# Performance work log

Measured on AMD Instinct MI355X. Metric: run time of the kernel, lower is better.

## Reference

```python
import math
import jax, jax.numpy as jnp
import numpy as np

N_HEADS = 16

def setup_inputs() -> dict:
    key = jax.random.key(0)
    ks = jax.random.split(key, 6)
    B, T, D = 2, 4096, 1024
    m, dh = 256, D // N_HEADS
    x = jax.random.normal(ks[0], (B, T, D), dtype=jnp.float32)
    s = 1.0 / math.sqrt(D)
    wq = jax.random.normal(ks[1], (D, D), dtype=jnp.float32) * s
    wk = jax.random.normal(ks[2], (D, D), dtype=jnp.float32) * s
    wv = jax.random.normal(ks[3], (D, D), dtype=jnp.float32) * s
    wo = jax.random.normal(ks[4], (D, D), dtype=jnp.float32) * s
    rf = jax.random.normal(ks[5], (m, dh), dtype=jnp.float32) / math.sqrt(dh)
    return {"x": x, "wq": wq, "wk": wk, "wv": wv, "wo": wo, "rf": rf}

def _phi(x, rf, m):
    # x: [B,H,T,Dh]; rf: [m,Dh] -> phi: [B,H,T,2m]
    norms_sq = jnp.sum(x * x, axis=-1, keepdims=True)            # [B,H,T,1]
    proj = jnp.einsum('bhtd,md->bhtm', x, rf)                     # [B,H,T,m]
    scale = jnp.exp(-norms_sq * 0.5) / math.sqrt(m)
    return jnp.concatenate([jnp.cos(proj), jnp.sin(proj)], axis=-1) * scale

def reference(x, wq, wk, wv, wo, rf):
    B, T, D = x.shape
    H = N_HEADS
    Dh = D // H
    m = rf.shape[0]
    def heads(w):
        return (x @ w.T).reshape(B, T, H, Dh).transpose(0, 2, 1, 3)  # [B,H,T,Dh]
    Q, K, V = heads(wq), heads(wk), heads(wv)
    Qf = _phi(Q, rf, m)                                            # [B,H,T,2m]
    Kf = _phi(K, rf, m)
    KV = jnp.einsum('bhnd,bhnv->bhdv', Kf, V)                      # [B,H,2m,Dh]
    QKV = jnp.einsum('bhnd,bhdv->bhnv', Qf, KV)                    # [B,H,T,Dh]
    K_sum = jnp.sum(Kf, axis=2)                                    # [B,H,2m]
    Z = jnp.maximum(jnp.einsum('bhnd,bhd->bhn', Qf, K_sum)[..., None], 1e-6)
    out = (QKV / Z).transpose(0, 2, 1, 3).reshape(B, T, D)
    return out @ wo.T
```

## Files before the change

kernel.cpp:

```cpp
#include <hip/hip_runtime.h>


#define TSEQ  4096
#define BSZ   2
#define BT    8192
#define DM    1024
#define NHEAD 16
#define DHEAD 64
#define FF    512

typedef __attribute__((ext_vector_type(8))) __bf16 bf16x8;
typedef __attribute__((ext_vector_type(4))) __bf16 bf16x4;
typedef __attribute__((ext_vector_type(4))) float floatx4;

#define MFMA_BF16(a, b, c) __builtin_amdgcn_mfma_f32_16x16x32_bf16(a, b, c, 0, 0, 0)

__device__ __forceinline__ void load_lds_16B(const void* g, void* l) {
    __builtin_amdgcn_global_load_lds(
        (const __attribute__((address_space(1))) void*)g,
        (__attribute__((address_space(3))) void*)l, 16, 0, 0);
}

__global__ __launch_bounds__(256) void split2_kernel(
    const float* __restrict__ src, __bf16* __restrict__ hi, __bf16* __restrict__ lo, int n4)
{
    int i = blockIdx.x * 256 + threadIdx.x;
    if (i >= n4) return;
    float4 v = ((const float4*)src)[i];
    bf16x4 h = {(__bf16)v.x, (__bf16)v.y, (__bf16)v.z, (__bf16)v.w};
    bf16x4 l = {(__bf16)(v.x - (float)h[0]), (__bf16)(v.y - (float)h[1]),
                (__bf16)(v.z - (float)h[2]), (__bf16)(v.w - (float)h[3])};
    ((bf16x4*)hi)[i] = h;
    ((bf16x4*)lo)[i] = l;
}

__global__ __launch_bounds__(256) void split1_kernel(
    const float* __restrict__ src, __bf16* __restrict__ hi, int n4)
{
    int i = blockIdx.x * 256 + threadIdx.x;
    if (i >= n4) return;
    float4 v = ((const float4*)src)[i];
    bf16x4 h = {(__bf16)v.x, (__bf16)v.y, (__bf16)v.z, (__bf16)v.w};
    ((bf16x4*)hi)[i] = h;
}

template<bool SPLIT, int EPI>
__global__ __launch_bounds__(256, 2)
void gemm_mfma_kernel(const __bf16* __restrict__ Ahi, const __bf16* __restrict__ Alo,
                      const __bf16* __restrict__ Whi, const __bf16* __restrict__ Wlo,
                      float* __restrict__ Cf, __bf16* __restrict__ Cb,
                      float* __restrict__ norms)
{
    __shared__ __bf16 As[SPLIT ? 2 : 1][128 * 32];
    __shared__ __bf16 Bs[SPLIT ? 2 : 1][128 * 32];

    const int t = threadIdx.x;
    const int bm = blockIdx.y * 128, bn = blockIdx.x * 128;
    const int lane = t & 63, mth = lane & 15, q = lane >> 4, wave = t >> 6;
    const int wrow = (wave & 1) * 64, wcol = (wave >> 1) * 64;
    const int qsw = q ^ ((mth >> 1) & 3);
    const int csw = (t & 3) ^ ((t >> 3) & 3);

    const size_t arow = (size_t)(bm + (t >> 2)) * DM + csw * 8;
    const size_t brow = (size_t)(bn + (t >> 2)) * DM + csw * 8;
    const int l0 = t * 8;
    const int l1 = 64 * 32 + t * 8;

    floatx4 acc[4][4];
#pragma unroll
    for (int i = 0; i < 4; ++i)
#pragma unroll
        for (int j = 0; j < 4; ++j) acc[i][j] = (floatx4){0.f, 0.f, 0.f, 0.f};

    for (int k0 = 0; k0 < DM; k0 += 32) {
        __syncthreads();
        load_lds_16B(Ahi + arow + k0,             &As[0][l0]);
        load_lds_16B(Ahi + arow + 64 * DM + k0,   &As[0][l1]);
        load_lds_16B(Whi + brow + k0,             &Bs[0][l0]);
        load_lds_16B(Whi + brow + 64 * DM + k0,   &Bs[0][l1]);
        if (SPLIT) {
            load_lds_16B(Alo + arow + k0,           &As[1][l0]);
            load_lds_16B(Alo + arow + 64 * DM + k0, &As[1][l1]);
            load_lds_16B(Wlo + brow + k0,           &Bs[1][l0]);
            load_lds_16B(Wlo + brow + 64 * DM + k0, &Bs[1][l1]);
        }
        __syncthreads();

        bf16x8 ah[4], bh[4], al[4], bl[4];
#pragma unroll
        for (int i = 0; i < 4; ++i) {
            ah[i] = *(const bf16x8*)&As[0][(wrow + i * 16 + mth) * 32 + qsw * 8];
            bh[i] = *(const bf16x8*)&Bs[0][(wcol + i * 16 + mth) * 32 + qsw * 8];
        }
        if (SPLIT) {
#pragma unroll
            for (int i = 0; i < 4; ++i) {
                al[i] = *(const bf16x8*)&As[1][(wrow + i * 16 + mth) * 32 + qsw * 8];
                bl[i] = *(const bf16x8*)&Bs[1][(wcol + i * 16 + mth) * 32 + qsw * 8];
            }
        }
#pragma unroll
        for (int i = 0; i < 4; ++i)
#pragma unroll
            for (int j = 0; j < 4; ++j) {
                acc[i][j] = MFMA_BF16(ah[i], bh[j], acc[i][j]);
                if (SPLIT) {
                    acc[i][j] = MFMA_BF16(ah[i], bl[j], acc[i][j]);
                    acc[i][j] = MFMA_BF16(al[i], bh[j], acc[i][j]);
                }
            }
    }

    if (EPI == 2) {
        const int head = (bn + wcol) >> 6;
#pragma unroll
        for (int i = 0; i < 4; ++i)
#pragma unroll
            for (int r = 0; r < 4; ++r) {
                float s = acc[i][0][r] * acc[i][0][r] + acc[i][1][r] * acc[i][1][r]
                        + acc[i][2][r] * acc[i][2][r] + acc[i][3][r] * acc[i][3][r];
                s += __shfl_xor(s, 1); s += __shfl_xor(s, 2);
                s += __shfl_xor(s, 4); s += __shfl_xor(s, 8);
                if (mth == 0)
                    norms[(size_t)head * BT + (bm + wrow + i * 16 + q * 4 + r)] = s;
            }
    }
    if (EPI == 3) {
#pragma unroll
        for (int i = 0; i < 4; ++i)
#pragma unroll
            for (int j = 0; j < 4; ++j) {
                const int cg = bn + wcol + j * 16 + mth;
                const int hh = cg >> 6, vloc = cg & 63;
                const int r0 = bm + wrow + i * 16 + q * 4;
                const int bb = r0 >> 12, tloc = r0 & 4095;
                bf16x4 w = {(__bf16)acc[i][j][0], (__bf16)acc[i][j][1],
                            (__bf16)acc[i][j][2], (__bf16)acc[i][j][3]};
                *(bf16x4*)(Cb + ((size_t)(bb * 16 + hh) * 64 + vloc) * TSEQ + tloc) = w;
            }
        return;
    }
#pragma unroll
    for (int i = 0; i < 4; ++i)
#pragma unroll
        for (int r = 0; r < 4; ++r) {
            const size_t gr = (size_t)(bm + wrow + i * 16 + q * 4 + r) * DM
                            + bn + wcol + mth;
            if (EPI == 0) {
#pragma unroll
                for (int j = 0; j < 4; ++j) Cf[gr + j * 16] = acc[i][j][r];
            } else {
#pragma unroll
                for (int j = 0; j < 4; ++j) Cb[gr + j * 16] = (__bf16)acc[i][j][r];
            }
        }
}

__global__ __launch_bounds__(256, 3)
void kv_mfma_kernel(const __bf16* __restrict__ Kb, const __bf16* __restrict__ Vt,
                    const float* __restrict__ Knorm,
                    const __bf16* __restrict__ rfh_g, const __bf16* __restrict__ rfl_g,
                    float* __restrict__ KVpart)
{
    __shared__ __bf16 rfh[4096], rfl[4096], Kc[4096], VtS[5120], phiT[8192];
    __shared__ float scaleS[64];

    const int fb = blockIdx.x, bh = blockIdx.y, z = blockIdx.z;
    const int b = bh >> 4, h = bh & 15;
    const int tid = threadIdx.x, wave = tid >> 6, lane = tid & 63;
    const int m = lane & 15, q = lane >> 4;
    const int lr = lane >> 2;
    const int csw = (lane & 3) ^ ((lr >> 1) & 3);
    const int qsw = q ^ ((m >> 1) & 3);

#pragma unroll
    for (int L = 0; L < 2; ++L) {
        const int f = wave * 16 + lr, d = L * 32 + csw * 8;
        load_lds_16B(rfh_g + (size_t)(fb * 64 + f) * DHEAD + d,
                     (char*)rfh + L * 4096 + wave * 1024 + lane * 16);
        load_lds_16B(rfl_g + (size_t)(fb * 64 + f) * DHEAD + d,
                     (char*)rfl + L * 4096 + wave * 1024 + lane * 16);
    }
    for (int idx = tid; idx < 1024; idx += 256) {
        const int kt = idx >> 9, rr = (idx >> 5) & 15, cc = idx & 31;
        VtS[kt * 2560 + (64 + rr) * 32 + cc] = (rr == 0) ? (__bf16)1.0f : (__bf16)0.0f;
    }

    floatx4 acc[2][5];
#pragma unroll
    for (int s = 0; s < 2; ++s)
#pragma unroll
        for (int v = 0; v < 5; ++v) acc[s][v] = (floatx4){0.f, 0.f, 0.f, 0.f};

    for (int ch = z * 8; ch < z * 8 + 8; ++ch) {
        __syncthreads();
#pragma unroll
        for (int L = 0; L < 2; ++L) {
            const int tr = wave * 16 + lr, d = L * 32 + csw * 8;
            load_lds_16B(Kb + (size_t)(b * TSEQ + ch * 64 + tr) * DM + h * 64 + d,
                         (char*)Kc + L * 4096 + wave * 1024 + lane * 16);
            load_lds_16B(Vt + ((size_t)bh * 64 + tr) * TSEQ + ch * 64 + d,
                         (char*)VtS + L * 5120 + wave * 1024 + lane * 16);
        }
        if (tid < 64)
            scaleS[tid] = __expf(-0.5f * Knorm[(size_t)h * BT + b * TSEQ + ch * 64 + tid]) * 0.0625f;
        __syncthreads();

        floatx4 pr[4];
#pragma unroll
        for (int ft = 0; ft < 4; ++ft) pr[ft] = (floatx4){0.f, 0.f, 0.f, 0.f};
#pragma unroll
        for (int kt = 0; kt < 2; ++kt) {
            const bf16x8 ka = *(const bf16x8*)(Kc + kt * 2048 + (wave * 16 + m) * 32 + qsw * 8);
#pragma unroll
            for (int ft = 0; ft < 4; ++ft) {
                const bf16x8 yh = *(const bf16x8*)(rfh + kt * 2048 + (ft * 16 + m) * 32 + qsw * 8);
                const bf16x8 yl = *(const bf16x8*)(rfl + kt * 2048 + (ft * 16 + m) * 32 + qsw * 8);
                pr[ft] = MFMA_BF16(ka, yh, pr[ft]);
                pr[ft] = MFMA_BF16(ka, yl, pr[ft]);
            }
        }
        {
            const int pg = wave >> 1;
            const int cph = (wave & 1) * 2 + (q >> 1);
            const int sub8 = (q & 1) * 8;
#pragma unroll
            for (int ft = 0; ft < 4; ++ft) {
                const int fo = ft * 16 + m;
                bf16x4 pc, ps;
#pragma unroll
                for (int r = 0; r < 4; ++r) {
                    const float sc = scaleS[wave * 16 + q * 4 + r];
                    float sv, cv;
                    __sincosf(pr[ft][r], &sv, &cv);
                    pc[r] = (__bf16)(cv * sc);
                    ps[r] = (__bf16)(sv * sc);
                }
                const int off = pg * 8192 + fo * 64 + (cph ^ ((m >> 1) & 3)) * 16 + sub8;
                *(bf16x4*)((char*)phiT + off) = pc;
                *(bf16x4*)((char*)phiT + off + 4096) = ps;
            }
        }
        __syncthreads();

#pragma unroll
        for (int kt = 0; kt < 2; ++kt) {
            bf16x8 yph[2];
#pragma unroll
            for (int f2 = 0; f2 < 2; ++f2)
                yph[f2] = *(const bf16x8*)((char*)phiT + kt * 8192
                          + (wave * 32 + f2 * 16 + m) * 64 + qsw * 16);
#pragma unroll
            for (int vt = 0; vt < 5; ++vt) {
                const bf16x8 xv = *(const bf16x8*)(VtS + kt * 2560 + (vt * 16 + m) * 32 + qsw * 8);
#pragma unroll
                for (int f2 = 0; f2 < 2; ++f2)
                    acc[f2][vt] = MFMA_BF16(xv, yph[f2], acc[f2][vt]);
            }
        }
    }

#pragma unroll
    for (int f2 = 0; f2 < 2; ++f2) {
        const int fo = wave * 32 + f2 * 16 + m;
        const int fg = (fo < 64) ? fb * 64 + fo : 256 + fb * 64 + (fo - 64);
#pragma unroll
        for (int vt = 0; vt < 5; ++vt) {
            float* base = KVpart + ((size_t)(z * 32 + bh) * 80 + vt * 16 + q * 4) * 512 + fg;
#pragma unroll
            for (int r = 0; r < 4; ++r) base[(size_t)r * 512] = acc[f2][vt][r];
        }
    }
}

#define KVTN (32 * 80 * 512)

__global__ __launch_bounds__(256) void reduce_kv_kernel(
    const float* __restrict__ KVpart, __bf16* __restrict__ KVthi)
{
    const int i = blockIdx.x * 256 + threadIdx.x;
    const float4* P = (const float4*)KVpart;
    float4 s = P[i];
#pragma unroll
    for (int j = 1; j < 8; ++j) {
        const float4 p = P[i + (size_t)j * (KVTN / 4)];
        s.x += p.x; s.y += p.y; s.z += p.z; s.w += p.w;
    }
    bf16x4 hv = {(__bf16)s.x, (__bf16)s.y, (__bf16)s.z, (__bf16)s.w};
    ((bf16x4*)KVthi)[i] = hv;
}

__global__ __launch_bounds__(256, 3)
void qkv_mfma_kernel(const __bf16* __restrict__ Qb, const float* __restrict__ Qnorm,
                     const __bf16* __restrict__ rfh_g, const __bf16* __restrict__ rfl_g,
                     const __bf16* __restrict__ KVthi, __bf16* __restrict__ Ybf)
{
    __shared__ __bf16 Qs[4096], uS[8192], KVh[10240];
    __shared__ float scaleS[128];

    const int tt = blockIdx.x, bh = blockIdx.y;
    const int b = bh >> 4, h = bh & 15;
    const int t0 = tt * 128;
    const int tid = threadIdx.x, wave = tid >> 6, lane = tid & 63;
    const int m = lane & 15, q = lane >> 4;
    const int lr = lane >> 2;
    const int csw = (lane & 3) ^ ((lr >> 1) & 3);
    const int qsw = q ^ ((m >> 1) & 3);

    if (tid < 128)
        scaleS[tid] = __expf(-0.5f * Qnorm[(size_t)h * BT + b * TSEQ + t0 + tid]) * 0.0625f;

    floatx4 acc[2][5];
#pragma unroll
    for (int s = 0; s < 2; ++s)
#pragma unroll
        for (int v = 0; v < 5; ++v) acc[s][v] = (floatx4){0.f, 0.f, 0.f, 0.f};

    for (int fb = 0; fb < 4; ++fb) {
        __syncthreads();
        {
            const int fgb = (wave < 2) ? fb * 64 + wave * 32 : 256 + fb * 64 + (wave - 2) * 32;
#pragma unroll
            for (int L = 0; L < 5; ++L) {
                const int v = L * 16 + lr;
                load_lds_16B(KVthi + ((size_t)bh * 80 + v) * 512 + fgb + csw * 8,
                             (char*)KVh + wave * 5120 + L * 1024 + lane * 16);
            }
        }
        for (int sub = 0; sub < 2; ++sub) {
            __syncthreads();
#pragma unroll
            for (int L = 0; L < 2; ++L) {
                const int tr = wave * 16 + lr, d = L * 32 + csw * 8;
                load_lds_16B(Qb + (size_t)(b * TSEQ + t0 + sub * 64 + tr) * DM + h * 64 + d,
                             (char*)Qs + L * 4096 + wave * 1024 + lane * 16);
                load_lds_16B(rfh_g + (size_t)(fb * 64 + tr) * DHEAD + d,
                             (char*)uS + L * 4096 + wave * 1024 + lane * 16);
                load_lds_16B(rfl_g + (size_t)(fb * 64 + tr) * DHEAD + d,
                             (char*)uS + 8192 + L * 4096 + wave * 1024 + lane * 16);
            }
            __syncthreads();

            floatx4 pr[4];
#pragma unroll
            for (int i = 0; i < 4; ++i) pr[i] = (floatx4){0.f, 0.f, 0.f, 0.f};
#pragma unroll
            for (int kt = 0; kt < 2; ++kt) {
                const bf16x8 xh = *(const bf16x8*)(uS + kt * 2048 + (wave * 16 + m) * 32 + qsw * 8);
                const bf16x8 xl = *(const bf16x8*)(uS + 4096 + kt * 2048 + (wave * 16 + m) * 32 + qsw * 8);
#pragma unroll
                for (int tt_ = 0; tt_ < 4; ++tt_) {
                    const bf16x8 yq = *(const bf16x8*)(Qs + kt * 2048 + (tt_ * 16 + m) * 32 + qsw * 8);
                    pr[tt_] = MFMA_BF16(xh, yq, pr[tt_]);
                    pr[tt_] = MFMA_BF16(xl, yq, pr[tt_]);
                }
            }
            __syncthreads();

            {
                const int pg = wave >> 1;
                const int cph = (wave & 1) * 2 + (q >> 1);
                const int sub8 = (q & 1) * 8;
#pragma unroll
                for (int tt_ = 0; tt_ < 4; ++tt_) {
                    const int tloc = tt_ * 16 + m;
                    const float sc = scaleS[sub * 64 + tloc];
                    bf16x4 pc, ps;
#pragma unroll
                    for (int r = 0; r < 4; ++r) {
                        float sv, cv;
                        __sincosf(pr[tt_][r], &sv, &cv);
                        pc[r] = (__bf16)(cv * sc);
                        ps[r] = (__bf16)(sv * sc);
                    }
                    const int off = pg * 4096 + tloc * 64 + (cph ^ ((m >> 1) & 3)) * 16 + sub8;
                    *(bf16x4*)((char*)uS + off) = pc;
                    *(bf16x4*)((char*)uS + off + 8192) = ps;
                }
            }
            __syncthreads();

#pragma unroll
            for (int ktf = 0; ktf < 4; ++ktf) {
                const bf16x8 yf = *(const bf16x8*)((char*)uS + ktf * 4096
                                  + (wave * 16 + m) * 64 + qsw * 16);
#pragma unroll
                for (int vt = 0; vt < 5; ++vt) {
                    const bf16x8 xh = *(const bf16x8*)(KVh + ktf * 2560 + (vt * 16 + m) * 32 + qsw * 8);
                    acc[sub][vt] = MFMA_BF16(xh, yf, acc[sub][vt]);
                }
            }
        }
    }
#pragma unroll
    for (int sub = 0; sub < 2; ++sub) {
        const float zv = __shfl(acc[sub][4][0], m);
        const float inv = 1.0f / fmaxf(zv, 1e-6f);
        const size_t tg = (size_t)(b * TSEQ + t0 + sub * 64 + wave * 16 + m);
#pragma unroll
        for (int vt = 0; vt < 4; ++vt) {
            bf16x4 w;
#pragma unroll
            for (int r = 0; r < 4; ++r) w[r] = (__bf16)(acc[sub][vt][r] * inv);
            *(bf16x4*)(Ybf + tg * DM + h * 64 + vt * 16 + q * 4) = w;
        }
    }
}

extern "C" void kernel_launch(void* const* d_in, const int* in_sizes, int n_in,
                              void* d_out, int out_size, void* d_ws, size_t ws_size,
                              hipStream_t stream)
{
    (void)in_sizes; (void)n_in; (void)out_size; (void)ws_size;
    const float* x  = (const float*)d_in[0];
    const float* wq = (const float*)d_in[1];
    const float* wk = (const float*)d_in[2];
    const float* wv = (const float*)d_in[3];
    const float* wo = (const float*)d_in[4];
    const float* rf = (const float*)d_in[5];
    float* out = (float*)d_out;

    const size_t MN = (size_t)BT * DM;
    const size_t WN = (size_t)DM * DM;
    const size_t RN = 256 * 64;

    __bf16* Qb    = (__bf16*)d_ws;
    __bf16* Kbf   = Qb   + MN;
    __bf16* Vtb   = Kbf  + MN;
    __bf16* Xhi   = Vtb  + MN;
    __bf16* Xlo   = Xhi  + MN;
    __bf16* Wqh   = Xlo  + MN;
    __bf16* Wql   = Wqh + WN;
    __bf16* Wkh   = Wql + WN;
    __bf16* Wkl   = Wkh + WN;
    __bf16* Wvh   = Wkl + WN;
    __bf16* Woh   = Wvh + WN;
    __bf16* rfhb  = Woh + WN;
    __bf16* rflb  = rfhb + RN;
    float* Qnorm  = (float*)(rflb + RN);
    float* Knorm  = Qnorm + (size_t)BT * NHEAD;
    __bf16* KVthi = (__bf16*)(Knorm + (size_t)BT * NHEAD);
    float* KVpart = (float*)Xhi;
    __bf16* Ybf   = Xhi;

    const dim3 blk(256);
    hipLaunchKernelGGL(split2_kernel, dim3(MN / 4 / 256), blk, 0, stream, x,  Xhi, Xlo, (int)(MN / 4));
    hipLaunchKernelGGL(split2_kernel, dim3(WN / 4 / 256), blk, 0, stream, wq, Wqh, Wql, (int)(WN / 4));
    hipLaunchKernelGGL(split2_kernel, dim3(WN / 4 / 256), blk, 0, stream, wk, Wkh, Wkl, (int)(WN / 4));
    hipLaunchKernelGGL(split1_kernel, dim3(WN / 4 / 256), blk, 0, stream, wv, Wvh, (int)(WN / 4));
    hipLaunchKernelGGL(split1_kernel, dim3(WN / 4 / 256), blk, 0, stream, wo, Woh, (int)(WN / 4));
    hipLaunchKernelGGL(split2_kernel, dim3(RN / 4 / 256), blk, 0, stream, rf, rfhb, rflb, (int)(RN / 4));

    const dim3 ggrid(DM / 128, BT / 128);
    hipLaunchKernelGGL((gemm_mfma_kernel<true, 2>), ggrid, blk, 0, stream,
                       Xhi, Xlo, Wqh, Wql, (float*)nullptr, Qb, Qnorm);
    hipLaunchKernelGGL((gemm_mfma_kernel<true, 2>), ggrid, blk, 0, stream,
                       Xhi, Xlo, Wkh, Wkl, (float*)nullptr, Kbf, Knorm);
    hipLaunchKernelGGL((gemm_mfma_kernel<false, 3>), ggrid, blk, 0, stream,
                       Xhi, (const __bf16*)nullptr, Wvh, (const __bf16*)nullptr,
                       (float*)nullptr, Vtb, (float*)nullptr);

    hipLaunchKernelGGL(kv_mfma_kernel, dim3(4, 32, 8), blk, 0, stream,
                       Kbf, Vtb, Knorm, rfhb, rflb, KVpart);
    hipLaunchKernelGGL(reduce_kv_kernel, dim3(KVTN / 4 / 256), blk, 0, stream,
                       KVpart, KVthi);
    hipLaunchKernelGGL(qkv_mfma_kernel, dim3(32, 32), blk, 0, stream,
                       Qb, Qnorm, rfhb, rflb, KVthi, Ybf);

    hipLaunchKernelGGL((gemm_mfma_kernel<false, 0>), ggrid, blk, 0, stream,
                       Ybf, (const __bf16*)nullptr, Woh, (const __bf16*)nullptr,
                       out, (__bf16*)nullptr, (float*)nullptr);
}
```

Before: 358.9 us.

## Fuse Q/K projections, merge weight splits, transpose V via LDS, restructure qkv loop

Merges the four weight-conversion launches into one kernel. Q and K projections become a single 512-thread kernel that shares the X hi/lo tiles across both weight matrices. The V-projection epilogue now transposes through LDS so the transposed stores are 16-byte vectors instead of 8-byte scattered writes. Grid axes are swapped so row blocks vary fastest. In the qkv kernel, the Q tile is loaded once, and the random-feature projection for both 64-row subtiles is done per feature block, which removes redundant reloads and syncs. The cost is more LDS per block and a higher register count in the fused GEMM, which may lower occupancy.

```diff
diff --git a/kernel.cpp b/kernel.cpp
--- a/kernel.cpp
+++ b/kernel.cpp
@@ -34,32 +34,129 @@
     ((bf16x4*)lo)[i] = l;
 }
 
-__global__ __launch_bounds__(256) void split1_kernel(
-    const float* __restrict__ src, __bf16* __restrict__ hi, int n4)
-{
-    int i = blockIdx.x * 256 + threadIdx.x;
-    if (i >= n4) return;
+__global__ __launch_bounds__(256) void split_weights_kernel(
+    const float* __restrict__ wq, const float* __restrict__ wk,
+    const float* __restrict__ wv, const float* __restrict__ wo,
+    const float* __restrict__ rf,
+    __bf16* __restrict__ Wqh, __bf16* __restrict__ Wql,
+    __bf16* __restrict__ Wkh, __bf16* __restrict__ Wkl,
+    __bf16* __restrict__ Wvh, __bf16* __restrict__ Woh,
+    __bf16* __restrict__ rfh, __bf16* __restrict__ rfl)
+{
+    const int id = blockIdx.x;
+    const float* src; __bf16* dh; __bf16* dl; int i;
+    if (id < 1024)      { src = wq; dh = Wqh; dl = Wql;     i = id * 256; }
+    else if (id < 2048) { src = wk; dh = Wkh; dl = Wkl;     i = (id - 1024) * 256; }
+    else if (id < 3072) { src = wv; dh = Wvh; dl = nullptr; i = (id - 2048) * 256; }
+    else if (id < 4096) { src = wo; dh = Woh; dl = nullptr; i = (id - 3072) * 256; }
+    else                { src = rf; dh = rfh; dl = rfl;     i = (id - 4096) * 256; }
+    i += threadIdx.x;
     float4 v = ((const float4*)src)[i];
     bf16x4 h = {(__bf16)v.x, (__bf16)v.y, (__bf16)v.z, (__bf16)v.w};
-    ((bf16x4*)hi)[i] = h;
-}
-
-template<bool SPLIT, int EPI>
+    ((bf16x4*)dh)[i] = h;
+    if (dl) {
+        bf16x4 l = {(__bf16)(v.x - (float)h[0]), (__bf16)(v.y - (float)h[1]),
+                    (__bf16)(v.z - (float)h[2]), (__bf16)(v.w - (float)h[3])};
+        ((bf16x4*)dl)[i] = l;
+    }
+}
+
+__global__ __launch_bounds__(512, 6)
+void gemm_qk_kernel(const __bf16* __restrict__ Ahi, const __bf16* __restrict__ Alo,
+                    const __bf16* __restrict__ Wqh, const __bf16* __restrict__ Wql,
+                    const __bf16* __restrict__ Wkh, const __bf16* __restrict__ Wkl,
+                    __bf16* __restrict__ Qb, __bf16* __restrict__ Kb,
+                    float* __restrict__ Qnorm, float* __restrict__ Knorm)
+{
+    __shared__ __bf16 As[2][4096];
+    __shared__ __bf16 Bq[2][4096];
+    __shared__ __bf16 Bk[2][4096];
+
+    const int t = threadIdx.x;
+    const int bm = blockIdx.x * 128, bn = blockIdx.y * 128;
+    const int lane = t & 63, mth = lane & 15, q = lane >> 4;
+    const int wave = t >> 6, grp = wave >> 2, wv = wave & 3;
+    const int wrow = (wv & 1) * 64, wcol = (wv >> 1) * 64;
+    const int qsw = q ^ ((mth >> 1) & 3);
+    const int row = t >> 2;
+    const int csw = (t & 3) ^ ((row >> 1) & 3);
+
+    const size_t arow = (size_t)(bm + row) * DM + csw * 8;
+    const size_t brow = (size_t)(bn + row) * DM + csw * 8;
+
+    floatx4 acc[4][4];
+#pragma unroll
+    for (int i = 0; i < 4; ++i)
+#pragma unroll
+        for (int j = 0; j < 4; ++j) acc[i][j] = (floatx4){0.f, 0.f, 0.f, 0.f};
+
+    const char* Bbase = grp ? (const char*)Bk : (const char*)Bq;
+
+    for (int k0 = 0; k0 < DM; k0 += 32) {
+        __syncthreads();
+        load_lds_16B(Ahi + arow + k0, (char*)As + t * 16);
+        load_lds_16B(Alo + arow + k0, (char*)As + 8192 + t * 16);
+        load_lds_16B(Wqh + brow + k0, (char*)Bq + t * 16);
+        load_lds_16B(Wql + brow + k0, (char*)Bq + 8192 + t * 16);
+        load_lds_16B(Wkh + brow + k0, (char*)Bk + t * 16);
+        load_lds_16B(Wkl + brow + k0, (char*)Bk + 8192 + t * 16);
+        __syncthreads();
+
+        bf16x8 ah[4], al[4], bh[4], bl[4];
+#pragma unroll
+        for (int i = 0; i < 4; ++i) {
+            const int ao = ((wrow + i * 16 + mth) * 32 + qsw * 8) * 2;
+            ah[i] = *(const bf16x8*)((const char*)As + ao);
+            al[i] = *(const bf16x8*)((const char*)As + 8192 + ao);
+            const int bo = ((wcol + i * 16 + mth) * 32 + qsw * 8) * 2;
+            bh[i] = *(const bf16x8*)(Bbase + bo);
+            bl[i] = *(const bf16x8*)(Bbase + 8192 + bo);
+        }
+#pragma unroll
+        for (int i = 0; i < 4; ++i)
+#pragma unroll
+            for (int j = 0; j < 4; ++j) {
+                acc[i][j] = MFMA_BF16(ah[i], bh[j], acc[i][j]);
+                acc[i][j] = MFMA_BF16(ah[i], bl[j], acc[i][j]);
+                acc[i][j] = MFMA_BF16(al[i], bh[j], acc[i][j]);
+            }
+    }
+
+    __bf16* Cb = grp ? Kb : Qb;
+    float* norms = grp ? Knorm : Qnorm;
+    const int head = (bn + wcol) >> 6;
+#pragma unroll
+    for (int i = 0; i < 4; ++i)
+#pragma unroll
+        for (int r = 0; r < 4; ++r) {
+            float s = acc[i][0][r] * acc[i][0][r] + acc[i][1][r] * acc[i][1][r]
+                    + acc[i][2][r] * acc[i][2][r] + acc[i][3][r] * acc[i][3][r];
+            s += __shfl_xor(s, 1); s += __shfl_xor(s, 2);
+            s += __shfl_xor(s, 4); s += __shfl_xor(s, 8);
+            const int grow = bm + wrow + i * 16 + q * 4 + r;
+            if (mth == 0) norms[(size_t)head * BT + grow] = s;
+            const size_t gr = (size_t)grow * DM + bn + wcol + mth;
+#pragma unroll
+            for (int j = 0; j < 4; ++j) Cb[gr + j * 16] = (__bf16)acc[i][j][r];
+        }
+}
+
+template<int EPI>
 __global__ __launch_bounds__(256, 2)
-void gemm_mfma_kernel(const __bf16* __restrict__ Ahi, const __bf16* __restrict__ Alo,
-                      const __bf16* __restrict__ Whi, const __bf16* __restrict__ Wlo,
-                      float* __restrict__ Cf, __bf16* __restrict__ Cb,
-                      float* __restrict__ norms)
-{
-    __shared__ __bf16 As[SPLIT ? 2 : 1][128 * 32];
-    __shared__ __bf16 Bs[SPLIT ? 2 : 1][128 * 32];
+void gemm_mfma_kernel(const __bf16* __restrict__ Ahi, const __bf16* __restrict__ Whi,
+                      float* __restrict__ Cf, __bf16* __restrict__ Cb)
+{
+    __shared__ __bf16 As[4096];
+    __shared__ __bf16 Bs[4096];
+    __shared__ __bf16 TrS[EPI == 3 ? 4 * 64 * 66 : 1];
 
     const int t = threadIdx.x;
-    const int bm = blockIdx.y * 128, bn = blockIdx.x * 128;
+    const int bm = blockIdx.x * 128, bn = blockIdx.y * 128;
     const int lane = t & 63, mth = lane & 15, q = lane >> 4, wave = t >> 6;
     const int wrow = (wave & 1) * 64, wcol = (wave >> 1) * 64;
     const int qsw = q ^ ((mth >> 1) & 3);
-    const int csw = (t & 3) ^ ((t >> 3) & 3);
+    const int row = t >> 2;
+    const int csw = (t & 3) ^ ((row >> 1) & 3);
 
     const size_t arow = (size_t)(bm + (t >> 2)) * DM + csw * 8;
     const size_t brow = (size_t)(bn + (t >> 2)) * DM + csw * 8;
@@ -74,70 +171,43 @@
 
     for (int k0 = 0; k0 < DM; k0 += 32) {
         __syncthreads();
-        load_lds_16B(Ahi + arow + k0,             &As[0][l0]);
-        load_lds_16B(Ahi + arow + 64 * DM + k0,   &As[0][l1]);
-        load_lds_16B(Whi + brow + k0,             &Bs[0][l0]);
-        load_lds_16B(Whi + brow + 64 * DM + k0,   &Bs[0][l1]);
-        if (SPLIT) {
-            load_lds_16B(Alo + arow + k0,           &As[1][l0]);
-            load_lds_16B(Alo + arow + 64 * DM + k0, &As[1][l1]);
-            load_lds_16B(Wlo + brow + k0,           &Bs[1][l0]);
-            load_lds_16B(Wlo + brow + 64 * DM + k0, &Bs[1][l1]);
-        }
-        __syncthreads();
-
-        bf16x8 ah[4], bh[4], al[4], bl[4];
+        load_lds_16B(Ahi + arow + k0,           &As[l0]);
+        load_lds_16B(Ahi + arow + 64 * DM + k0, &As[l1]);
+        load_lds_16B(Whi + brow + k0,           &Bs[l0]);
+        load_lds_16B(Whi + brow + 64 * DM + k0, &Bs[l1]);
+        __syncthreads();
+
+        bf16x8 ah[4], bh[4];
 #pragma unroll
         for (int i = 0; i < 4; ++i) {
-            ah[i] = *(const bf16x8*)&As[0][(wrow + i * 16 + mth) * 32 + qsw * 8];
-            bh[i] = *(const bf16x8*)&Bs[0][(wcol + i * 16 + mth) * 32 + qsw * 8];
-        }
-        if (SPLIT) {
-#pragma unroll
-            for (int i = 0; i < 4; ++i) {
-                al[i] = *(const bf16x8*)&As[1][(wrow + i * 16 + mth) * 32 + qsw * 8];
-                bl[i] = *(const bf16x8*)&Bs[1][(wcol + i * 16 + mth) * 32 + qsw * 8];
-            }
+            ah[i] = *(const bf16x8*)&As[(wrow + i * 16 + mth) * 32 + qsw * 8];
+            bh[i] = *(const bf16x8*)&Bs[(wcol + i * 16 + mth) * 32 + qsw * 8];
         }
 #pragma unroll
         for (int i = 0; i < 4; ++i)
 #pragma unroll
+            for (int j = 0; j < 4; ++j)
+                acc[i][j] = MFMA_BF16(ah[i], bh[j], acc[i][j]);
+    }
+
+    if (EPI == 3) {
+        __bf16* Tr = TrS + wave * (64 * 66);
+#pragma unroll
+        for (int i = 0; i < 4; ++i)
+#pragma unroll
             for (int j = 0; j < 4; ++j) {
-                acc[i][j] = MFMA_BF16(ah[i], bh[j], acc[i][j]);
-                if (SPLIT) {
-                    acc[i][j] = MFMA_BF16(ah[i], bl[j], acc[i][j]);
-                    acc[i][j] = MFMA_BF16(al[i], bh[j], acc[i][j]);
-                }
-            }
-    }
-
-    if (EPI == 2) {
-        const int head = (bn + wcol) >> 6;
-#pragma unroll
-        for (int i = 0; i < 4; ++i)
-#pragma unroll
-            for (int r = 0; r < 4; ++r) {
-                float s = acc[i][0][r] * acc[i][0][r] + acc[i][1][r] * acc[i][1][r]
-                        + acc[i][2][r] * acc[i][2][r] + acc[i][3][r] * acc[i][3][r];
-                s += __shfl_xor(s, 1); s += __shfl_xor(s, 2);
-                s += __shfl_xor(s, 4); s += __shfl_xor(s, 8);
-                if (mth == 0)
-                    norms[(size_t)head * BT + (bm + wrow + i * 16 + q * 4 + r)] = s;
-            }
-    }
-    if (EPI == 3) {
-#pragma unroll
-        for (int i = 0; i < 4; ++i)
-#pragma unroll
-            for (int j = 0; j < 4; ++j) {
-                const int cg = bn + wcol + j * 16 + mth;
-                const int hh = cg >> 6, vloc = cg & 63;
-                const int r0 = bm + wrow + i * 16 + q * 4;
-                const int bb = r0 >> 12, tloc = r0 & 4095;
                 bf16x4 w = {(__bf16)acc[i][j][0], (__bf16)acc[i][j][1],
                             (__bf16)acc[i][j][2], (__bf16)acc[i][j][3]};
-                *(bf16x4*)(Cb + ((size_t)(bb * 16 + hh) * 64 + vloc) * TSEQ + tloc) = w;
-            }
+                *(bf16x4*)(Tr + (j * 16 + mth) * 66 + i * 16 + q * 4) = w;
+            }
+        const int cg = bn + wcol + lane;
+        const int hh = cg >> 6, vloc = cg & 63;
+        const int r0 = bm + wrow;
+        const int bb = r0 >> 12, tloc = r0 & 4095;
+        __bf16* dst = Cb + ((size_t)(bb * 16 + hh) * 64 + vloc) * TSEQ + tloc;
+#pragma unroll
+        for (int k = 0; k < 8; ++k)
+            *(bf16x8*)(dst + k * 8) = *(const bf16x8*)(Tr + lane * 66 + k * 8);
         return;
     }
 #pragma unroll
@@ -146,13 +216,8 @@
         for (int r = 0; r < 4; ++r) {
             const size_t gr = (size_t)(bm + wrow + i * 16 + q * 4 + r) * DM
                             + bn + wcol + mth;
-            if (EPI == 0) {
-#pragma unroll
-                for (int j = 0; j < 4; ++j) Cf[gr + j * 16] = acc[i][j][r];
-            } else {
-#pragma unroll
-                for (int j = 0; j < 4; ++j) Cb[gr + j * 16] = (__bf16)acc[i][j][r];
-            }
+#pragma unroll
+            for (int j = 0; j < 4; ++j) Cf[gr + j * 16] = acc[i][j][r];
         }
 }
 
@@ -295,7 +360,10 @@
                      const __bf16* __restrict__ rfh_g, const __bf16* __restrict__ rfl_g,
                      const __bf16* __restrict__ KVthi, __bf16* __restrict__ Ybf)
 {
-    __shared__ __bf16 Qs[4096], uS[8192], KVh[10240];
+    __shared__ __bf16 Qs[8192];
+    __shared__ __bf16 uS[8192];
+    __shared__ __bf16 uS2[8192];
+    __shared__ __bf16 KVh[10240];
     __shared__ float scaleS[128];
 
     const int tt = blockIdx.x, bh = blockIdx.y;
@@ -304,12 +372,22 @@
     const int tid = threadIdx.x, wave = tid >> 6, lane = tid & 63;
     const int m = lane & 15, q = lane >> 4;
     const int lr = lane >> 2;
-    const int csw = (lane & 3) ^ ((lr >> 1) & 3);
+    const int cswl = (lane & 3) ^ ((lr >> 1) & 3);
     const int qsw = q ^ ((m >> 1) & 3);
+    const int trq = tid >> 2;
+    const int cswq = (tid & 3) ^ ((trq >> 1) & 3);
 
     if (tid < 128)
         scaleS[tid] = __expf(-0.5f * Qnorm[(size_t)h * BT + b * TSEQ + t0 + tid]) * 0.0625f;
 
+#pragma unroll
+    for (int p = 0; p < 4; ++p) {
+        const int sub = p >> 1, kt = p & 1;
+        load_lds_16B(Qb + (size_t)(b * TSEQ + t0 + sub * 64 + trq) * DM + h * 64
+                        + kt * 32 + cswq * 8,
+                     (char*)Qs + p * 4096 + tid * 16);
+    }
+
     floatx4 acc[2][5];
 #pragma unroll
     for (int s = 0; s < 2; ++s)
@@ -318,45 +396,48 @@
 
     for (int fb = 0; fb < 4; ++fb) {
         __syncthreads();
+#pragma unroll
+        for (int p = 0; p < 2; ++p) {
+            load_lds_16B(rfh_g + (size_t)(fb * 64 + trq) * DHEAD + p * 32 + cswq * 8,
+                         (char*)uS + p * 4096 + tid * 16);
+            load_lds_16B(rfl_g + (size_t)(fb * 64 + trq) * DHEAD + p * 32 + cswq * 8,
+                         (char*)uS2 + p * 4096 + tid * 16);
+        }
         {
             const int fgb = (wave < 2) ? fb * 64 + wave * 32 : 256 + fb * 64 + (wave - 2) * 32;
 #pragma unroll
             for (int L = 0; L < 5; ++L) {
                 const int v = L * 16 + lr;
-                load_lds_16B(KVthi + ((size_t)bh * 80 + v) * 512 + fgb + csw * 8,
+                load_lds_16B(KVthi + ((size_t)bh * 80 + v) * 512 + fgb + cswl * 8,
                              (char*)KVh + wave * 5120 + L * 1024 + lane * 16);
             }
         }
+        __syncthreads();
+
+        floatx4 pr[2][4];
+#pragma unroll
+        for (int s = 0; s < 2; ++s)
+#pragma unroll
+            for (int i = 0; i < 4; ++i) pr[s][i] = (floatx4){0.f, 0.f, 0.f, 0.f};
+#pragma unroll
+        for (int kt = 0; kt < 2; ++kt) {
+            const int xo = kt * 4096 + ((wave * 16 + m) * 32 + qsw * 8) * 2;
+            const bf16x8 xh = *(const bf16x8*)((const char*)uS + xo);
+            const bf16x8 xl = *(const bf16x8*)((const char*)uS2 + xo);
+#pragma unroll
+            for (int sub = 0; sub < 2; ++sub)
+#pragma unroll
+                for (int tt_ = 0; tt_ < 4; ++tt_) {
+                    const bf16x8 yq = *(const bf16x8*)((const char*)Qs + (sub * 2 + kt) * 4096
+                                      + ((tt_ * 16 + m) * 32 + qsw * 8) * 2);
+                    pr[sub][tt_] = MFMA_BF16(xh, yq, pr[sub][tt_]);
+                    pr[sub][tt_] = MFMA_BF16(xl, yq, pr[sub][tt_]);
+                }
+        }
+        __syncthreads();
+
+#pragma unroll
         for (int sub = 0; sub < 2; ++sub) {
-            __syncthreads();
-#pragma unroll
-            for (int L = 0; L < 2; ++L) {
-                const int tr = wave * 16 + lr, d = L * 32 + csw * 8;
-                load_lds_16B(Qb + (size_t)(b * TSEQ + t0 + sub * 64 + tr) * DM + h * 64 + d,
-                             (char*)Qs + L * 4096 + wave * 1024 + lane * 16);
-                load_lds_16B(rfh_g + (size_t)(fb * 64 + tr) * DHEAD + d,
-                             (char*)uS + L * 4096 + wave * 1024 + lane * 16);
-                load_lds_16B(rfl_g + (size_t)(fb * 64 + tr) * DHEAD + d,
-                             (char*)uS + 8192 + L * 4096 + wave * 1024 + lane * 16);
-            }
-            __syncthreads();
-
-            floatx4 pr[4];
-#pragma unroll
-            for (int i = 0; i < 4; ++i) pr[i] = (floatx4){0.f, 0.f, 0.f, 0.f};
-#pragma unroll
-            for (int kt = 0; kt < 2; ++kt) {
-                const bf16x8 xh = *(const bf16x8*)(uS + kt * 2048 + (wave * 16 + m) * 32 + qsw * 8);
-                const bf16x8 xl = *(const bf16x8*)(uS + 4096 + kt * 2048 + (wave * 16 + m) * 32 + qsw * 8);
-#pragma unroll
-                for (int tt_ = 0; tt_ < 4; ++tt_) {
-                    const bf16x8 yq = *(const bf16x8*)(Qs + kt * 2048 + (tt_ * 16 + m) * 32 + qsw * 8);
-                    pr[tt_] = MFMA_BF16(xh, yq, pr[tt_]);
-                    pr[tt_] = MFMA_BF16(xl, yq, pr[tt_]);
-                }
-            }
-            __syncthreads();
-
             {
                 const int pg = wave >> 1;
                 const int cph = (wave & 1) * 2 + (q >> 1);
@@ -369,27 +450,29 @@
 #pragma unroll
                     for (int r = 0; r < 4; ++r) {
                         float sv, cv;
-                        __sincosf(pr[tt_][r], &sv, &cv);
+                        __sincosf(pr[sub][tt_][r], &sv, &cv);
                         pc[r] = (__bf16)(cv * sc);
                         ps[r] = (__bf16)(sv * sc);
                     }
                     const int off = pg * 4096 + tloc * 64 + (cph ^ ((m >> 1) & 3)) * 16 + sub8;
                     *(bf16x4*)((char*)uS + off) = pc;
-                    *(bf16x4*)((char*)uS + off + 8192) = ps;
+                    *(bf16x4*)((char*)uS2 + off) = ps;
                 }
             }
             __syncthreads();
 
 #pragma unroll
             for (int ktf = 0; ktf < 4; ++ktf) {
-                const bf16x8 yf = *(const bf16x8*)((char*)uS + ktf * 4096
-                                  + (wave * 16 + m) * 64 + qsw * 16);
+                const char* phip = (ktf < 2) ? (const char*)uS + ktf * 4096
+                                             : (const char*)uS2 + (ktf - 2) * 4096;
+                const bf16x8 yf = *(const bf16x8*)(phip + (wave * 16 + m) * 64 + qsw * 16);
 #pragma unroll
                 for (int vt = 0; vt < 5; ++vt) {
                     const bf16x8 xh = *(const bf16x8*)(KVh + ktf * 2560 + (vt * 16 + m) * 32 + qsw * 8);
                     acc[sub][vt] = MFMA_BF16(xh, yf, acc[sub][vt]);
                 }
             }
+            if (sub == 0) __syncthreads();
         }
     }
 #pragma unroll
@@ -444,21 +527,15 @@
     __bf16* Ybf   = Xhi;
 
     const dim3 blk(256);
-    hipLaunchKernelGGL(split2_kernel, dim3(MN / 4 / 256), blk, 0, stream, x,  Xhi, Xlo, (int)(MN / 4));
-    hipLaunchKernelGGL(split2_kernel, dim3(WN / 4 / 256), blk, 0, stream, wq, Wqh, Wql, (int)(WN / 4));
-    hipLaunchKernelGGL(split2_kernel, dim3(WN / 4 / 256), blk, 0, stream, wk, Wkh, Wkl, (int)(WN / 4));
-    hipLaunchKernelGGL(split1_kernel, dim3(WN / 4 / 256), blk, 0, stream, wv, Wvh, (int)(WN / 4));
-    hipLaunchKernelGGL(split1_kernel, dim3(WN / 4 / 256), blk, 0, stream, wo, Woh, (int)(WN / 4));
-    hipLaunchKernelGGL(split2_kernel, dim3(RN / 4 / 256), blk, 0, stream, rf, rfhb, rflb, (int)(RN / 4));
-
-    const dim3 ggrid(DM / 128, BT / 128);
-    hipLaunchKernelGGL((gemm_mfma_kernel<true, 2>), ggrid, blk, 0, stream,
-                       Xhi, Xlo, Wqh, Wql, (float*)nullptr, Qb, Qnorm);
-    hipLaunchKernelGGL((gemm_mfma_kernel<true, 2>), ggrid, blk, 0, stream,
-                       Xhi, Xlo, Wkh, Wkl, (float*)nullptr, Kbf, Knorm);
-    hipLaunchKernelGGL((gemm_mfma_kernel<false, 3>), ggrid, blk, 0, stream,
-                       Xhi, (const __bf16*)nullptr, Wvh, (const __bf16*)nullptr,
-                       (float*)nullptr, Vtb, (float*)nullptr);
+    hipLaunchKernelGGL(split2_kernel, dim3(MN / 4 / 256), blk, 0, stream,
+                       x, Xhi, Xlo, (int)(MN / 4));
+    hipLaunchKernelGGL(split_weights_kernel, dim3(4096 + RN / 4 / 256), blk, 0, stream,
+                       wq, wk, wv, wo, rf, Wqh, Wql, Wkh, Wkl, Wvh, Woh, rfhb, rflb);
+
+    hipLaunchKernelGGL(gemm_qk_kernel, dim3(64, 8), dim3(512), 0, stream,
+                       Xhi, Xlo, Wqh, Wql, Wkh, Wkl, Qb, Kbf, Qnorm, Knorm);
+    hipLaunchKernelGGL((gemm_mfma_kernel<3>), dim3(64, 8), blk, 0, stream,
+                       Xhi, Wvh, (float*)nullptr, Vtb);
 
     hipLaunchKernelGGL(kv_mfma_kernel, dim3(4, 32, 8), blk, 0, stream,
                        Kbf, Vtb, Knorm, rfhb, rflb, KVpart);
@@ -467,7 +544,6 @@
     hipLaunchKernelGGL(qkv_mfma_kernel, dim3(32, 32), blk, 0, stream,
                        Qb, Qnorm, rfhb, rflb, KVthi, Ybf);
 
-    hipLaunchKernelGGL((gemm_mfma_kernel<false, 0>), ggrid, blk, 0, stream,
-                       Ybf, (const __bf16*)nullptr, Woh, (const __bf16*)nullptr,
-                       out, (__bf16*)nullptr, (float*)nullptr);
-}
+    hipLaunchKernelGGL((gemm_mfma_kernel<0>), dim3(64, 8), blk, 0, stream,
+                       Ybf, Woh, out, (__bf16*)nullptr);
+}
```

After: 1.033 ms. 2.88x slower.
